# Performance work log

Measured on AMD Instinct MI355X. Metric: run time of the kernel, lower is better.

Reference implementation:

```python
import jax, jax.numpy as jnp
import numpy as np

NQ = 64
BIG = 1e10

FILTERS = np.array([[1,0,0,1,0,0,1,0,0],
                    [0,0,0,0,0,0,1,1,1],
                    [0,0,1,0,0,1,0,0,1],
                    [1,1,1,0,0,0,0,0,0],
                    [0,0,0,1,0,0,1,1,0],
                    [0,0,0,0,0,1,0,1,1],
                    [0,1,1,0,0,1,0,0,0],
                    [1,1,0,1,0,0,0,0,0]], dtype=np.float32).reshape(8,1,3,3)


def _conv2d(x, k):
    return jax.lax.conv_general_dilated(x, k, (1,1), 'SAME',
                                        dimension_numbers=('NCHW','OIHW','NCHW'))


def _maxpool3(x):  # 3x3 stride-1 maxpool, pad=1 (pads with -inf like torch)
    return jax.lax.reduce_window(x, -jnp.inf, jax.lax.max, (1,1,3,3), (1,1,1,1), 'SAME')


def setup_inputs() -> dict:
    key = jax.random.key(0)
    ks = jax.random.split(key, 5)
    b, h, w = 2, 240, 320
    n = 2 * h * w  # 153600 points
    fx = fy = 300.0
    cx, cy = w / 2.0, h / 2.0
    z  = jax.random.uniform(ks[0], (b, n), minval=1.0, maxval=10.0)
    u  = jax.random.uniform(ks[1], (b, n), minval=0.0, maxval=float(w))
    v  = jax.random.uniform(ks[2], (b, n), minval=0.0, maxval=float(h))
    xw = (u - cx) / fx * z
    yw = (v - cy) / fy * z
    rgb = jax.random.uniform(ks[3], (b, 3, n))
    pp = jnp.concatenate([xw[:, None], yw[:, None], z[:, None],
                          jnp.ones((b, 1, n), jnp.float32), rgb], axis=1)  # [b,7,n]
    conf = jax.random.uniform(ks[4], (b, n))
    pose_w2c = jnp.tile(jnp.eye(4, dtype=jnp.float32)[None], (b, 1, 1))
    K = jnp.tile(jnp.array([[fx, 0, cx], [0, fy, cy], [0, 0, 1.0]], jnp.float32)[None], (b, 1, 1))
    filters = jnp.asarray(FILTERS)
    return {"pp": pp, "conf": conf, "pose_w2c": pose_w2c, "K": K,
            "filters": filters, "h": h, "w": w}


def reference(pp, conf, pose_w2c, K, filters, h, w,
              znear=0.1, zfar=1000.0, conf_thresh=0.0):
    b, _, n = pp.shape
    # world -> camera (wsz=1 so the hi-res pool is identity)
    pc = jnp.einsum('bij,bjn->bin', pose_w2c, pp[:, :4])          # [b,4,n]
    z  = jnp.abs(pc[:, 2])                                        # [b,n]
    xc = pc[:, 0] * K[:, 0, 0][:, None] / z + K[:, 0, 2][:, None]
    yc = pc[:, 1] * K[:, 1, 1][:, None] / z + K[:, 1, 2][:, None]
    x = jnp.round(xc).astype(jnp.int32)
    y = jnp.round(yc).astype(jnp.int32)
    oob = ((x < 0) | (x >= w) | (y < 0) | (y >= h) |
           (z < znear) | (z > zfar) | (conf <= conf_thresh))
    # inverse-depth quantization bounds over valid points only
    inv_lo = 1.0 / jnp.where(oob, 1e-10, z)   # oob -> 1e10, drops out of min
    inv_hi = 1.0 / jnp.where(oob, BIG, z)     # oob -> 1e-10, drops out of max
    dmin = jnp.min(inv_lo, axis=-1, keepdims=True)
    dmax = jnp.max(inv_hi, axis=-1, keepdims=True)
    do = ((inv_hi - dmin) / (dmax - dmin) * (NQ - 1)).astype(jnp.int32)  # [b,n]

    # scatter points into [b, NQ, h, w] z-buffer bins (drop invalid)
    size = b * NQ * h * w
    bidx = jnp.arange(b, dtype=jnp.int32)[:, None]
    idx = ((bidx * NQ + do) * h + y) * w + x
    idx = jnp.where(oob, size, idx).reshape(-1)   # 'size' is out of bounds -> dropped
    zf = z.astype(jnp.float32).reshape(-1)
    dmap = jnp.zeros((size,), jnp.float32).at[idx].set(zf, mode='drop').reshape(b, NQ, h, w)
    cmap = jnp.full((size,), -1.0, jnp.float32).at[idx].set(conf.reshape(-1), mode='drop').reshape(b, NQ, h, w)
    rgb_pts = pp[:, 4:].transpose(0, 2, 1).reshape(-1, 3).astype(jnp.float32)
    rgb = jnp.zeros((size, 3), jnp.float32).at[idx].set(rgb_pts, mode='drop').reshape(b, NQ, h, w, 3)

    # z-buffer composite: nearest non-empty bin per pixel
    dmap = jnp.where(dmap <= 0, BIG, dmap)
    min_idx = jnp.argmin(dmap, axis=1)                             # [b,h,w]
    dflat = jnp.min(dmap, axis=1)
    dflat = jnp.where(dflat >= BIG, 0.0, dflat)
    cflat = jnp.take_along_axis(cmap, min_idx[:, None], axis=1)[:, 0]
    cflat = jnp.maximum(cflat, 0.0)                                # cmap_[cmap_<0]=0
    rflat = jnp.take_along_axis(rgb, min_idx[:, None, :, :, None], axis=1)[:, 0]  # [b,h,w,3]

    # vertical flip (torch.flip over h)
    depths = dflat[:, ::-1][:, None]                               # [b,1,h,w]
    confs  = cflat[:, ::-1][:, None]
    rgbs   = jnp.transpose(rflat[:, ::-1], (0, 3, 1, 2))           # [b,3,h,w]

    # hole filling: 2 iterations of oriented-filter tests + 3x3 max pooling
    ones_k = jnp.ones((1, 1, 3, 3), jnp.float32)
    for _ in range(2):
        tofill = (_conv2d(depths, ones_k) > 0) & (depths <= 0)
        o = _conv2d(depths, filters)                               # [b,8,h,w]
        fill = (jnp.abs(jnp.prod(o, axis=1, keepdims=True)) > 1e-10) & tofill
        f = fill.astype(jnp.float32)
        depths = depths * (1 - f) + f * _maxpool3(depths)
        confs  = confs  * (1 - f) + f * _maxpool3(confs)
        rgbs   = rgbs   * (1 - f) + f * _maxpool3(rgbs)
    return depths, confs, rgbs
```

## Files before the change

kernel.cpp:

```cpp
#include <hip/hip_runtime.h>
#include <stdint.h>

#define NQ 64
#define ZNEAR 0.1f
#define ZFAR 1000.0f
#define FT 16

__device__ __forceinline__ float wave_min_f(float v) {
    #pragma unroll
    for (int off = 1; off < 64; off <<= 1)
        v = fminf(v, __shfl_xor(v, off, 64));
    return v;
}
__device__ __forceinline__ float wave_max_f(float v) {
    #pragma unroll
    for (int off = 1; off < 64; off <<= 1)
        v = fmaxf(v, __shfl_xor(v, off, 64));
    return v;
}

__global__ void k_project(const float* __restrict__ pp, const float* __restrict__ conf,
                          const float* __restrict__ pose, const float* __restrict__ Km,
                          const int* __restrict__ hp, const int* __restrict__ wp,
                          int B, int n,
                          float* __restrict__ zbuf, unsigned* __restrict__ packed,
                          float4* __restrict__ zcr8,
                          float* __restrict__ pmin, float* __restrict__ pmax, int nBlk,
                          unsigned* __restrict__ pixwin, int pixTot) {
    int bb = blockIdx.y;
    int i = blockIdx.x * blockDim.x + threadIdx.x;
    size_t ztid = ((size_t)blockIdx.y * gridDim.x + blockIdx.x) * blockDim.x + threadIdx.x;
    if (ztid < (size_t)pixTot) pixwin[ztid] = 0u;

    int h = *hp, w = *wp;
    float inv_lo = INFINITY;
    float inv_hi = 0.0f;
    if (i < n) {
        const float* P  = pose + (size_t)bb * 16;
        const float* km = Km   + (size_t)bb * 9;
        const float* pb = pp   + (size_t)bb * 7 * n;
        float X  = pb[0 * (size_t)n + i];
        float Y  = pb[1 * (size_t)n + i];
        float Z  = pb[2 * (size_t)n + i];
        float Wc = pb[3 * (size_t)n + i];
        float pc0 = P[0] * X + P[1] * Y + P[2]  * Z + P[3]  * Wc;
        float pc1 = P[4] * X + P[5] * Y + P[6]  * Z + P[7]  * Wc;
        float pc2 = P[8] * X + P[9] * Y + P[10] * Z + P[11] * Wc;
        float z = fabsf(pc2);
        float xc = pc0 * km[0] / z + km[2];
        float yc = pc1 * km[4] / z + km[5];
        float xr = rintf(xc);
        float yr = rintf(yc);
        float cf = conf[(size_t)bb * n + i];
        bool valid = (xr >= 0.0f) && (xr <= (float)(w - 1)) &&
                     (yr >= 0.0f) && (yr <= (float)(h - 1)) &&
                     (z >= ZNEAR) && (z <= ZFAR) && (cf > 0.0f);
        unsigned px = valid ? (unsigned)(int)xr : 0u;
        unsigned py = valid ? (unsigned)(int)yr : 0u;
        size_t p = (size_t)bb * n + i;
        zbuf[p] = z;
        packed[p] = (valid ? 0x80000000u : 0u) | px | (py << 12);
        zcr8[2 * p]     = make_float4(z, cf, pb[4 * (size_t)n + i], pb[5 * (size_t)n + i]);
        zcr8[2 * p + 1] = make_float4(pb[6 * (size_t)n + i], 0.0f, 0.0f, 0.0f);
        inv_lo = valid ? (1.0f / z) : (1.0f / 1e-10f);
        inv_hi = valid ? (1.0f / z) : (1.0f / 1e10f);
    }
    __shared__ float smin[4], smax[4];
    float wmin = wave_min_f(inv_lo);
    float wmax = wave_max_f(inv_hi);
    int lane = threadIdx.x & 63, wid = threadIdx.x >> 6;
    if (lane == 0) { smin[wid] = wmin; smax[wid] = wmax; }
    __syncthreads();
    if (threadIdx.x == 0) {
        pmin[(size_t)bb * nBlk + blockIdx.x] = fminf(fminf(smin[0], smin[1]), fminf(smin[2], smin[3]));
        pmax[(size_t)bb * nBlk + blockIdx.x] = fmaxf(fmaxf(smax[0], smax[1]), fmaxf(smax[2], smax[3]));
    }
}

__global__ void k_scatter(const float* __restrict__ zbuf, const unsigned* __restrict__ packed,
                          const float* __restrict__ pminb, const float* __restrict__ pmaxb, int nBlk,
                          const int* __restrict__ hp, const int* __restrict__ wp,
                          int B, int n, unsigned* __restrict__ pixwin) {
    __shared__ float smin[4], smax[4];
    __shared__ float sdlo[8], sdhi[8];
    for (int bb = 0; bb < B; ++bb) {
        float lmin = INFINITY, lmax = 0.0f;
        for (int k = threadIdx.x; k < nBlk; k += blockDim.x) {
            lmin = fminf(lmin, pminb[(size_t)bb * nBlk + k]);
            lmax = fmaxf(lmax, pmaxb[(size_t)bb * nBlk + k]);
        }
        lmin = wave_min_f(lmin);
        lmax = wave_max_f(lmax);
        int lane = threadIdx.x & 63, wid = threadIdx.x >> 6;
        if (lane == 0) { smin[wid] = lmin; smax[wid] = lmax; }
        __syncthreads();
        if (threadIdx.x == 0) {
            sdlo[bb] = fminf(fminf(smin[0], smin[1]), fminf(smin[2], smin[3]));
            sdhi[bb] = fmaxf(fmaxf(smax[0], smax[1]), fmaxf(smax[2], smax[3]));
        }
        __syncthreads();
    }
    int p = blockIdx.x * blockDim.x + threadIdx.x;
    if (p >= B * n) return;
    unsigned pk = packed[p];
    if (!(pk & 0x80000000u)) return;
    int bb = p / n;
    int i = p - bb * n;
    float inv = 1.0f / zbuf[p];
    float dlo = sdlo[bb], dhi = sdhi[bb];
    int dq = (int)((inv - dlo) / (dhi - dlo) * (float)(NQ - 1));
    int h = *hp, w = *wp;
    int x = (int)(pk & 0xFFFu);
    int y = (int)((pk >> 12) & 0xFFFu);
    unsigned key = ((unsigned)dq << 20) | (unsigned)(i + 1);
    atomicMax(&pixwin[(size_t)bb * h * w + (size_t)y * w + x], key);
}

__global__ void __launch_bounds__(256, 4)
k_resfill(const float4* __restrict__ zcr8, const unsigned* __restrict__ pixwin,
          const float* __restrict__ filt,
          const int* __restrict__ hp, const int* __restrict__ wp,
          int B, int n, float* __restrict__ out, int pixTot) {
    int h = *hp, w = *wp;
    int tilesX = (w + FT - 1) / FT;
    int tilesY = (h + FT - 1) / FT;
    int TPB = tilesX * tilesY;
    int T = TPB * B;
    int hw = h * w;
    int tid = threadIdx.x;

    __shared__ float s_f[72];
    __shared__ float s_in[5][20][20];
    __shared__ float s_m[5][18][18];
    if (tid < 72) s_f[tid] = filt[tid];

    for (int t = blockIdx.x; t < T; t += gridDim.x) {
        int bb = t / TPB;
        int tile = t - bb * TPB;
        int tY = tile / tilesX, tX = tile - tY * tilesX;
        int gy0 = tY * FT - 2, gx0 = tX * FT - 2;

        for (int idx = tid; idx < 400; idx += blockDim.x) {
            int yy = idx / 20, xx = idx - yy * 20;
            int gy = gy0 + yy, gx = gx0 + xx;
            float v0 = 0.0f, v1 = 0.0f, v2 = 0.0f, v3 = 0.0f, v4 = 0.0f;
            if (((unsigned)gy < (unsigned)h) && ((unsigned)gx < (unsigned)w)) {
                int ys = h - 1 - gy;
                unsigned key = pixwin[(size_t)bb * hw + (size_t)ys * w + gx];
                if (key) {
                    int i = (int)(key & 0xFFFFFu) - 1;
                    size_t p = (size_t)bb * n + i;
                    float4 a = zcr8[2 * p];
                    float4 c = zcr8[2 * p + 1];
                    v0 = a.x; v1 = a.y; v2 = a.z; v3 = a.w; v4 = c.x;
                }
            }
            s_in[0][yy][xx] = v0;
            s_in[1][yy][xx] = v1;
            s_in[2][yy][xx] = v2;
            s_in[3][yy][xx] = v3;
            s_in[4][yy][xx] = v4;
        }
        __syncthreads();

        for (int idx = tid; idx < 324; idx += blockDim.x) {
            int py = idx / 18, px = idx - py * 18;
            int sy = py + 1, sx = px + 1;
            int gy = gy0 + sy, gx = gx0 + sx;
            bool vc = ((unsigned)gy < (unsigned)h) && ((unsigned)gx < (unsigned)w);
            float d[9];
            #pragma unroll
            for (int t9 = 0; t9 < 9; ++t9) d[t9] = s_in[0][sy + t9 / 3 - 1][sx + t9 % 3 - 1];
            float s = 0.0f;
            #pragma unroll
            for (int t9 = 0; t9 < 9; ++t9) s += d[t9];
            float dc0 = d[4];
            float ov[5];
            #pragma unroll
            for (int ch = 0; ch < 5; ++ch) ov[ch] = s_in[ch][sy][sx];
            if ((s > 0.0f) && (dc0 <= 0.0f)) {
                float prod = 1.0f;
                #pragma unroll
                for (int k = 0; k < 8; ++k) {
                    float o = 0.0f;
                    #pragma unroll
                    for (int t9 = 0; t9 < 9; ++t9) o += s_f[k * 9 + t9] * d[t9];
                    prod *= o;
                }
                if (fabsf(prod) > 1e-10f) {
                    #pragma unroll
                    for (int ch = 0; ch < 5; ++ch) {
                        float m = -INFINITY;
                        #pragma unroll
                        for (int t9 = 0; t9 < 9; ++t9) {
                            int ny = gy + t9 / 3 - 1, nx = gx + t9 % 3 - 1;
                            if (((unsigned)ny < (unsigned)h) && ((unsigned)nx < (unsigned)w))
                                m = fmaxf(m, s_in[ch][sy + t9 / 3 - 1][sx + t9 % 3 - 1]);
                        }
                        ov[ch] = m;
                    }
                }
            }
            if (!vc) { ov[0] = 0.0f; ov[1] = 0.0f; ov[2] = 0.0f; ov[3] = 0.0f; ov[4] = 0.0f; }
            #pragma unroll
            for (int ch = 0; ch < 5; ++ch) s_m[ch][py][px] = ov[ch];
        }
        __syncthreads();

        int ly = tid >> 4, lx = tid & 15;
        int gy = tY * FT + ly, gx = tX * FT + lx;
        if (((unsigned)gy < (unsigned)h) && ((unsigned)gx < (unsigned)w)) {
            int sy = ly + 1, sx = lx + 1;
            float d[9];
            #pragma unroll
            for (int t9 = 0; t9 < 9; ++t9) d[t9] = s_m[0][sy + t9 / 3 - 1][sx + t9 % 3 - 1];
            float s = 0.0f;
            #pragma unroll
            for (int t9 = 0; t9 < 9; ++t9) s += d[t9];
            float dc0 = d[4];
            float ov[5];
            #pragma unroll
            for (int ch = 0; ch < 5; ++ch) ov[ch] = s_m[ch][sy][sx];
            if ((s > 0.0f) && (dc0 <= 0.0f)) {
                float prod = 1.0f;
                #pragma unroll
                for (int k = 0; k < 8; ++k) {
                    float o = 0.0f;
                    #pragma unroll
                    for (int t9 = 0; t9 < 9; ++t9) o += s_f[k * 9 + t9] * d[t9];
                    prod *= o;
                }
                if (fabsf(prod) > 1e-10f) {
                    #pragma unroll
                    for (int ch = 0; ch < 5; ++ch) {
                        float m = -INFINITY;
                        #pragma unroll
                        for (int t9 = 0; t9 < 9; ++t9) {
                            int ny = gy + t9 / 3 - 1, nx = gx + t9 % 3 - 1;
                            if (((unsigned)ny < (unsigned)h) && ((unsigned)nx < (unsigned)w))
                                m = fmaxf(m, s_m[ch][sy + t9 / 3 - 1][sx + t9 % 3 - 1]);
                        }
                        ov[ch] = m;
                    }
                }
            }
            size_t g = (size_t)gy * w + gx;
            out[(size_t)bb * hw + g] = ov[0];
            out[(size_t)pixTot + (size_t)bb * hw + g] = ov[1];
            size_t rb = 2 * (size_t)pixTot;
            out[rb + (((size_t)bb * 3 + 0) * hw) + g] = ov[2];
            out[rb + (((size_t)bb * 3 + 1) * hw) + g] = ov[3];
            out[rb + (((size_t)bb * 3 + 2) * hw) + g] = ov[4];
        }
    }
}

static inline size_t align32(size_t x) { return (x + 31) & ~(size_t)31; }

extern "C" void kernel_launch(void* const* d_in, const int* in_sizes, int n_in,
                              void* d_out, int out_size, void* d_ws, size_t ws_size,
                              hipStream_t stream) {
    const float* pp   = (const float*)d_in[0];
    const float* conf = (const float*)d_in[1];
    const float* pose = (const float*)d_in[2];
    const float* Km   = (const float*)d_in[3];
    const float* filt = (const float*)d_in[4];
    const int*   hp   = (const int*)d_in[5];
    const int*   wp   = (const int*)d_in[6];

    int B = in_sizes[2] / 16;
    int n = in_sizes[1] / B;
    size_t pix = (size_t)out_size / 5;
    size_t npts = (size_t)B * n;

    const int bs = 256;
    int nBlk = (n + bs - 1) / bs;

    char* ws = (char*)d_ws;
    size_t off = 0;
    unsigned* pixwin = (unsigned*)(ws + off); off = align32(off + pix * 4);
    float4* zcr8  = (float4*)(ws + off);      off = align32(off + npts * 32);
    float* zbuf   = (float*)(ws + off);       off = align32(off + npts * 4);
    unsigned* packed = (unsigned*)(ws + off); off = align32(off + npts * 4);
    float* pminb  = (float*)(ws + off);       off = align32(off + (size_t)B * nBlk * 4);
    float* pmaxb  = (float*)(ws + off);       off = align32(off + (size_t)B * nBlk * 4);

    float* out = (float*)d_out;
    int pixI = (int)pix;

    dim3 gproj(nBlk, B);
    k_project<<<gproj, bs, 0, stream>>>(pp, conf, pose, Km, hp, wp, B, n,
                                        zbuf, packed, zcr8, pminb, pmaxb, nBlk,
                                        pixwin, pixI);

    int nptsI = (int)npts;
    k_scatter<<<(nptsI + bs - 1) / bs, bs, 0, stream>>>(zbuf, packed, pminb, pmaxb, nBlk,
                                                        hp, wp, B, n, pixwin);

    k_resfill<<<1024, bs, 0, stream>>>(zcr8, pixwin, filt, hp, wp, B, n, out, pixI);
}
```

Measured before the change: 105.4 us.

## Fuse project, scatter and hole-fill into one cooperative kernel with grid syncs

Merges the three kernels into a single cooperative launch of 512 persistent blocks, using grid.sync between the projection/min-max stage, the atomic depth scatter and the tiled hole-filling stage. The goal is to remove inter-kernel launch gaps and to read the per-block min/max partials in place. In exchange the grid is fixed at 512 blocks with 2-per-CU launch bounds, which may lower occupancy in the fill stage. Grid-wide barriers also add their own cost.

```diff
diff --git a/kernel.cpp b/kernel.cpp
--- a/kernel.cpp
+++ b/kernel.cpp
@@ -1,10 +1,14 @@
 #include <hip/hip_runtime.h>
+#include <hip/hip_cooperative_groups.h>
 #include <stdint.h>
+
+namespace cg = cooperative_groups;
 
 #define NQ 64
 #define ZNEAR 0.1f
 #define ZFAR 1000.0f
 #define FT 16
+#define GRID_BLOCKS 512
 
 __device__ __forceinline__ float wave_min_f(float v) {
     #pragma unroll
@@ -19,119 +23,116 @@
     return v;
 }
 
-__global__ void k_project(const float* __restrict__ pp, const float* __restrict__ conf,
-                          const float* __restrict__ pose, const float* __restrict__ Km,
-                          const int* __restrict__ hp, const int* __restrict__ wp,
-                          int B, int n,
-                          float* __restrict__ zbuf, unsigned* __restrict__ packed,
-                          float4* __restrict__ zcr8,
-                          float* __restrict__ pmin, float* __restrict__ pmax, int nBlk,
-                          unsigned* __restrict__ pixwin, int pixTot) {
-    int bb = blockIdx.y;
-    int i = blockIdx.x * blockDim.x + threadIdx.x;
-    size_t ztid = ((size_t)blockIdx.y * gridDim.x + blockIdx.x) * blockDim.x + threadIdx.x;
-    if (ztid < (size_t)pixTot) pixwin[ztid] = 0u;
-
+__global__ void __launch_bounds__(256, 2)
+k_fused(const float* __restrict__ pp, const float* __restrict__ conf,
+        const float* __restrict__ pose, const float* __restrict__ Km,
+        const float* __restrict__ filt,
+        const int* __restrict__ hp, const int* __restrict__ wp,
+        int B, int n,
+        float* __restrict__ zbuf, unsigned* __restrict__ packed, float4* __restrict__ zcr8,
+        float* __restrict__ pminb, float* __restrict__ pmaxb,
+        unsigned* __restrict__ pixwin, float* __restrict__ out, int pixTot) {
+    cg::grid_group grid = cg::this_grid();
     int h = *hp, w = *wp;
-    float inv_lo = INFINITY;
-    float inv_hi = 0.0f;
-    if (i < n) {
+    int hw = h * w;
+    int nBlk = gridDim.x;
+    int tid = threadIdx.x;
+    int lane = tid & 63, wid = tid >> 6;
+
+    __shared__ float smin[4], smax[4];
+    __shared__ float sdlo[8], sdhi[8];
+    __shared__ float s_f[72];
+    __shared__ float s_in[5][20][20];
+    __shared__ float s_m[5][18][18];
+
+    for (size_t k = (size_t)blockIdx.x * blockDim.x + tid; k < (size_t)pixTot;
+         k += (size_t)gridDim.x * blockDim.x)
+        pixwin[k] = 0u;
+
+    for (int bb = 0; bb < B; ++bb) {
         const float* P  = pose + (size_t)bb * 16;
         const float* km = Km   + (size_t)bb * 9;
         const float* pb = pp   + (size_t)bb * 7 * n;
-        float X  = pb[0 * (size_t)n + i];
-        float Y  = pb[1 * (size_t)n + i];
-        float Z  = pb[2 * (size_t)n + i];
-        float Wc = pb[3 * (size_t)n + i];
-        float pc0 = P[0] * X + P[1] * Y + P[2]  * Z + P[3]  * Wc;
-        float pc1 = P[4] * X + P[5] * Y + P[6]  * Z + P[7]  * Wc;
-        float pc2 = P[8] * X + P[9] * Y + P[10] * Z + P[11] * Wc;
-        float z = fabsf(pc2);
-        float xc = pc0 * km[0] / z + km[2];
-        float yc = pc1 * km[4] / z + km[5];
-        float xr = rintf(xc);
-        float yr = rintf(yc);
-        float cf = conf[(size_t)bb * n + i];
-        bool valid = (xr >= 0.0f) && (xr <= (float)(w - 1)) &&
-                     (yr >= 0.0f) && (yr <= (float)(h - 1)) &&
-                     (z >= ZNEAR) && (z <= ZFAR) && (cf > 0.0f);
-        unsigned px = valid ? (unsigned)(int)xr : 0u;
-        unsigned py = valid ? (unsigned)(int)yr : 0u;
-        size_t p = (size_t)bb * n + i;
-        zbuf[p] = z;
-        packed[p] = (valid ? 0x80000000u : 0u) | px | (py << 12);
-        zcr8[2 * p]     = make_float4(z, cf, pb[4 * (size_t)n + i], pb[5 * (size_t)n + i]);
-        zcr8[2 * p + 1] = make_float4(pb[6 * (size_t)n + i], 0.0f, 0.0f, 0.0f);
-        inv_lo = valid ? (1.0f / z) : (1.0f / 1e-10f);
-        inv_hi = valid ? (1.0f / z) : (1.0f / 1e10f);
-    }
-    __shared__ float smin[4], smax[4];
-    float wmin = wave_min_f(inv_lo);
-    float wmax = wave_max_f(inv_hi);
-    int lane = threadIdx.x & 63, wid = threadIdx.x >> 6;
-    if (lane == 0) { smin[wid] = wmin; smax[wid] = wmax; }
-    __syncthreads();
-    if (threadIdx.x == 0) {
-        pmin[(size_t)bb * nBlk + blockIdx.x] = fminf(fminf(smin[0], smin[1]), fminf(smin[2], smin[3]));
-        pmax[(size_t)bb * nBlk + blockIdx.x] = fmaxf(fmaxf(smax[0], smax[1]), fmaxf(smax[2], smax[3]));
-    }
-}
-
-__global__ void k_scatter(const float* __restrict__ zbuf, const unsigned* __restrict__ packed,
-                          const float* __restrict__ pminb, const float* __restrict__ pmaxb, int nBlk,
-                          const int* __restrict__ hp, const int* __restrict__ wp,
-                          int B, int n, unsigned* __restrict__ pixwin) {
-    __shared__ float smin[4], smax[4];
-    __shared__ float sdlo[8], sdhi[8];
+        float lmin = INFINITY;
+        float lmax = 0.0f;
+        for (int i = blockIdx.x * blockDim.x + tid; i < n; i += gridDim.x * blockDim.x) {
+            float X  = pb[0 * (size_t)n + i];
+            float Y  = pb[1 * (size_t)n + i];
+            float Z  = pb[2 * (size_t)n + i];
+            float Wc = pb[3 * (size_t)n + i];
+            float pc0 = P[0] * X + P[1] * Y + P[2]  * Z + P[3]  * Wc;
+            float pc1 = P[4] * X + P[5] * Y + P[6]  * Z + P[7]  * Wc;
+            float pc2 = P[8] * X + P[9] * Y + P[10] * Z + P[11] * Wc;
+            float z = fabsf(pc2);
+            float xc = pc0 * km[0] / z + km[2];
+            float yc = pc1 * km[4] / z + km[5];
+            float xr = rintf(xc);
+            float yr = rintf(yc);
+            float cf = conf[(size_t)bb * n + i];
+            bool valid = (xr >= 0.0f) && (xr <= (float)(w - 1)) &&
+                         (yr >= 0.0f) && (yr <= (float)(h - 1)) &&
+                         (z >= ZNEAR) && (z <= ZFAR) && (cf > 0.0f);
+            unsigned px = valid ? (unsigned)(int)xr : 0u;
+            unsigned py = valid ? (unsigned)(int)yr : 0u;
+            size_t p = (size_t)bb * n + i;
+            zbuf[p] = z;
+            packed[p] = (valid ? 0x80000000u : 0u) | px | (py << 12);
+            zcr8[2 * p]     = make_float4(z, cf, pb[4 * (size_t)n + i], pb[5 * (size_t)n + i]);
+            zcr8[2 * p + 1] = make_float4(pb[6 * (size_t)n + i], 0.0f, 0.0f, 0.0f);
+            float inv_lo = valid ? (1.0f / z) : (1.0f / 1e-10f);
+            float inv_hi = valid ? (1.0f / z) : (1.0f / 1e10f);
+            lmin = fminf(lmin, inv_lo);
+            lmax = fmaxf(lmax, inv_hi);
+        }
+        float wmin = wave_min_f(lmin);
+        float wmax = wave_max_f(lmax);
+        if (lane == 0) { smin[wid] = wmin; smax[wid] = wmax; }
+        __syncthreads();
+        if (tid == 0) {
+            pminb[(size_t)bb * nBlk + blockIdx.x] = fminf(fminf(smin[0], smin[1]), fminf(smin[2], smin[3]));
+            pmaxb[(size_t)bb * nBlk + blockIdx.x] = fmaxf(fmaxf(smax[0], smax[1]), fmaxf(smax[2], smax[3]));
+        }
+        __syncthreads();
+    }
+
+    grid.sync();
+
     for (int bb = 0; bb < B; ++bb) {
         float lmin = INFINITY, lmax = 0.0f;
-        for (int k = threadIdx.x; k < nBlk; k += blockDim.x) {
+        for (int k = tid; k < nBlk; k += blockDim.x) {
             lmin = fminf(lmin, pminb[(size_t)bb * nBlk + k]);
             lmax = fmaxf(lmax, pmaxb[(size_t)bb * nBlk + k]);
         }
         lmin = wave_min_f(lmin);
         lmax = wave_max_f(lmax);
-        int lane = threadIdx.x & 63, wid = threadIdx.x >> 6;
         if (lane == 0) { smin[wid] = lmin; smax[wid] = lmax; }
         __syncthreads();
-        if (threadIdx.x == 0) {
+        if (tid == 0) {
             sdlo[bb] = fminf(fminf(smin[0], smin[1]), fminf(smin[2], smin[3]));
             sdhi[bb] = fmaxf(fmaxf(smax[0], smax[1]), fmaxf(smax[2], smax[3]));
         }
         __syncthreads();
     }
-    int p = blockIdx.x * blockDim.x + threadIdx.x;
-    if (p >= B * n) return;
-    unsigned pk = packed[p];
-    if (!(pk & 0x80000000u)) return;
-    int bb = p / n;
-    int i = p - bb * n;
-    float inv = 1.0f / zbuf[p];
-    float dlo = sdlo[bb], dhi = sdhi[bb];
-    int dq = (int)((inv - dlo) / (dhi - dlo) * (float)(NQ - 1));
-    int h = *hp, w = *wp;
-    int x = (int)(pk & 0xFFFu);
-    int y = (int)((pk >> 12) & 0xFFFu);
-    unsigned key = ((unsigned)dq << 20) | (unsigned)(i + 1);
-    atomicMax(&pixwin[(size_t)bb * h * w + (size_t)y * w + x], key);
-}
-
-__global__ void __launch_bounds__(256, 4)
-k_resfill(const float4* __restrict__ zcr8, const unsigned* __restrict__ pixwin,
-          const float* __restrict__ filt,
-          const int* __restrict__ hp, const int* __restrict__ wp,
-          int B, int n, float* __restrict__ out, int pixTot) {
-    int h = *hp, w = *wp;
+    for (int p = blockIdx.x * blockDim.x + tid; p < B * n; p += gridDim.x * blockDim.x) {
+        unsigned pk = packed[p];
+        if (!(pk & 0x80000000u)) continue;
+        int bb = p / n;
+        int i = p - bb * n;
+        float inv = 1.0f / zbuf[p];
+        float dlo = sdlo[bb], dhi = sdhi[bb];
+        int dq = (int)((inv - dlo) / (dhi - dlo) * (float)(NQ - 1));
+        int x = (int)(pk & 0xFFFu);
+        int y = (int)((pk >> 12) & 0xFFFu);
+        unsigned key = ((unsigned)dq << 20) | (unsigned)(i + 1);
+        atomicMax(&pixwin[(size_t)bb * hw + (size_t)y * w + x], key);
+    }
+
+    grid.sync();
+
     int tilesX = (w + FT - 1) / FT;
     int tilesY = (h + FT - 1) / FT;
     int TPB = tilesX * tilesY;
     int T = TPB * B;
-    int hw = h * w;
-    int tid = threadIdx.x;
-
-    __shared__ float s_f[72];
-    __shared__ float s_in[5][20][20];
-    __shared__ float s_m[5][18][18];
     if (tid < 72) s_f[tid] = filt[tid];
 
     for (int t = blockIdx.x; t < T; t += gridDim.x) {
@@ -139,6 +140,7 @@
         int tile = t - bb * TPB;
         int tY = tile / tilesX, tX = tile - tY * tilesX;
         int gy0 = tY * FT - 2, gx0 = tX * FT - 2;
+        __syncthreads();
 
         for (int idx = tid; idx < 400; idx += blockDim.x) {
             int yy = idx / 20, xx = idx - yy * 20;
@@ -273,29 +275,21 @@
     size_t pix = (size_t)out_size / 5;
     size_t npts = (size_t)B * n;
 
-    const int bs = 256;
-    int nBlk = (n + bs - 1) / bs;
-
     char* ws = (char*)d_ws;
     size_t off = 0;
     unsigned* pixwin = (unsigned*)(ws + off); off = align32(off + pix * 4);
     float4* zcr8  = (float4*)(ws + off);      off = align32(off + npts * 32);
     float* zbuf   = (float*)(ws + off);       off = align32(off + npts * 4);
     unsigned* packed = (unsigned*)(ws + off); off = align32(off + npts * 4);
-    float* pminb  = (float*)(ws + off);       off = align32(off + (size_t)B * nBlk * 4);
-    float* pmaxb  = (float*)(ws + off);       off = align32(off + (size_t)B * nBlk * 4);
+    float* pminb  = (float*)(ws + off);       off = align32(off + (size_t)GRID_BLOCKS * 8 * 4);
+    float* pmaxb  = (float*)(ws + off);       off = align32(off + (size_t)GRID_BLOCKS * 8 * 4);
 
     float* out = (float*)d_out;
     int pixI = (int)pix;
 
-    dim3 gproj(nBlk, B);
-    k_project<<<gproj, bs, 0, stream>>>(pp, conf, pose, Km, hp, wp, B, n,
-                                        zbuf, packed, zcr8, pminb, pmaxb, nBlk,
-                                        pixwin, pixI);
-
-    int nptsI = (int)npts;
-    k_scatter<<<(nptsI + bs - 1) / bs, bs, 0, stream>>>(zbuf, packed, pminb, pmaxb, nBlk,
-                                                        hp, wp, B, n, pixwin);
-
-    k_resfill<<<1024, bs, 0, stream>>>(zcr8, pixwin, filt, hp, wp, B, n, out, pixI);
-}
+    void* args[] = { (void*)&pp, (void*)&conf, (void*)&pose, (void*)&Km, (void*)&filt,
+                     (void*)&hp, (void*)&wp, (void*)&B, (void*)&n,
+                     (void*)&zbuf, (void*)&packed, (void*)&zcr8,
+                     (void*)&pminb, (void*)&pmaxb, (void*)&pixwin, (void*)&out, (void*)&pixI };
+    hipLaunchCooperativeKernel((void*)k_fused, dim3(GRID_BLOCKS), dim3(256), args, 0, stream);
+}
```

Measured after the change: 249.3 us. 136% more time.
